# Optimization experiments

Measured on AMD Instinct MI355X. Metric: run time of the kernel, lower is better.

Reference implementation:

```python
import jax, jax.numpy as jnp
import numpy as np

B, N_CAPS, N_VOTES, D_IN, D_H, D_CP = 1024, 64, 36, 256, 128, 32
TWO_PI = 2.0 * np.pi


def geometric_transform(pose):
    # pose: [..., 6] -> affine 3x3 matrix [..., 3, 3] (nonlinear, full affine)
    sx, sy, theta, shear, tx, ty = jnp.split(pose, 6, axis=-1)
    sx = jax.nn.sigmoid(sx) + 1e-2
    sy = jax.nn.sigmoid(sy) + 1e-2
    tx = jnp.tanh(tx * 5.0)
    ty = jnp.tanh(ty * 5.0)
    shear = jnp.tanh(shear * 5.0)
    theta = theta * TWO_PI
    c, s = jnp.cos(theta), jnp.sin(theta)
    row0 = jnp.concatenate([sx * c + shear * sy * s, -sx * s + shear * sy * c, tx], -1)
    row1 = jnp.concatenate([sy * s, sy * c, ty], -1)
    zeros = jnp.zeros_like(tx)
    row2 = jnp.concatenate([zeros, zeros, jnp.ones_like(tx)], -1)
    return jnp.stack([row0, row1, row2], axis=-2)


def setup_inputs() -> dict:
    key = jax.random.key(0)
    ks = jax.random.split(key, 16)
    u = lambda k, shp: 0.5 * (jax.random.uniform(k, shp, jnp.float32) - 0.5)
    return {
        "features": jax.random.normal(ks[0], (B, N_CAPS, D_IN), jnp.float32),
        "w1": u(ks[1], (1, N_CAPS, D_IN, D_H)),
        "b1": jnp.zeros((1, N_CAPS, 1, D_H), jnp.float32),
        "w2": u(ks[2], (1, N_CAPS, D_H, D_CP)),
        "b2": jnp.zeros((1, N_CAPS, 1, D_CP), jnp.float32),
        "caps_mlp_w": u(ks[3], (1, N_CAPS, D_CP + 1, D_H)),
        "caps_mlp_b": jnp.zeros((1, N_CAPS, 1, D_H), jnp.float32),
        "cpr_dynamic_w": u(ks[4], (1, N_CAPS, D_H, N_VOTES * 6)),
        "ccr_w": u(ks[5], (1, N_CAPS, D_H, 6)),
        "ccr_b": jnp.zeros((1, N_CAPS, 1, 6), jnp.float32),
        "pres_caps_w": u(ks[6], (1, N_CAPS, D_H, 1)),
        "pres_caps_b": jnp.zeros((1, N_CAPS, 1, 1), jnp.float32),
        "pres_vote_w": u(ks[7], (1, N_CAPS, D_H, N_VOTES)),
        "pres_vote_b": jnp.zeros((1, N_CAPS, 1, N_VOTES), jnp.float32),
        "scale_vote_w": u(ks[8], (1, N_CAPS, D_H, N_VOTES)),
        "scale_vote_b": jnp.zeros((1, N_CAPS, 1, N_VOTES), jnp.float32),
        "cpr_static": jax.random.uniform(ks[9], (1, N_CAPS, N_VOTES, 6), jnp.float32) - 0.5,
    }


def reference(features, w1, b1, w2, b2, caps_mlp_w, caps_mlp_b, cpr_dynamic_w,
              ccr_w, ccr_b, pres_caps_w, pres_caps_b, pres_vote_w, pres_vote_b,
              scale_vote_w, scale_vote_b, cpr_static):
    batch_size = features.shape[0]
    x = features[:, :, None, :]                               # [B, C, 1, 256]
    h = jax.nn.relu(x @ w1 + b1)                              # [B, C, 1, H]
    raw_caps_params = jax.nn.relu(h @ w2 + b2)                # [B, C, 1, P]
    caps_exist = jnp.ones(raw_caps_params.shape[:-1] + (1,), raw_caps_params.dtype)
    caps_params = jnp.concatenate([raw_caps_params, caps_exist], -1)  # [B, C, 1, P+1]
    caps_feat = jax.nn.relu(caps_params @ caps_mlp_w + caps_mlp_b)    # [B, C, 1, H]

    cpr_dynamic = (caps_feat @ cpr_dynamic_w).reshape(batch_size, N_CAPS, N_VOTES, 6)
    ccr = caps_feat @ ccr_w + ccr_b                           # [B, C, 1, 6]
    pres_logit_per_caps = (caps_feat @ pres_caps_w + pres_caps_b)[:, :, 0, :]   # [B, C, 1]
    pres_logit_per_vote = (caps_feat @ pres_vote_w + pres_vote_b)[:, :, 0, :]   # [B, C, V]
    scale_per_vote = (caps_feat @ scale_vote_w + scale_vote_b)[:, :, 0, :]      # [B, C, V]

    ccr_mat = geometric_transform(ccr)                        # [B, C, 1, 3, 3]
    cpr_mat = geometric_transform(cpr_dynamic + cpr_static)   # [B, C, V, 3, 3]
    votes = ccr_mat @ cpr_mat                                 # [B, C, V, 3, 3]

    pres_per_caps = jax.nn.sigmoid(pres_logit_per_caps)
    pres_per_vote = pres_per_caps * jax.nn.sigmoid(pres_logit_per_vote)
    scale_per_vote = jax.nn.softplus(scale_per_vote + 0.5) + 0.01
    dynamic_weights_l2 = jnp.sum(cpr_dynamic ** 2) / batch_size / 2.0
    return (votes, scale_per_vote, pres_per_vote, pres_logit_per_caps,
            pres_logit_per_vote, dynamic_weights_l2, raw_caps_params[:, :, 0, :], features)
```

## Files before the change

### kernel.cpp

```cpp
#include <hip/hip_runtime.h>
#include <math.h>

#define NB   1024
#define NC   64
#define DIN  256
#define DH   128
#define DCP  32
#define NV   36

#define OFF0 0
#define OFF1 21233664
#define OFF2 23592960
#define OFF3 25952256
#define OFF4 26017792
#define OFF5 28377088
#define OFF6 28377089
#define OFF7 30474241

#define SM_FST 0
#define SM_R2  4224
#define SM_R3  8576
#define SM_TOT 9664

#define SM_XS  SM_R2
#define SM_W1C (SM_R2 + 544)
#define SM_W2S SM_R2
#define SM_WM  SM_R2
#define SM_WH  SM_R2
#define SM_HD  (SM_R2 + 1280)
#define SM_HB  (SM_R2 + 3872)
#define SM_WD  SM_R2
#define SM_DYN SM_R2
#define SM_CPS SM_R3
#define SM_M   SM_R3
#define SM_PSIG (SM_R3 + 192)

__device__ __forceinline__ float sigm(float x) { return 1.0f / (1.0f + __expf(-x)); }
__device__ __forceinline__ float tanh5(float x) {
    x = fminf(fmaxf(5.0f * x, -15.0f), 15.0f);
    float z = __expf(2.0f * x);
    return (z - 1.0f) / (z + 1.0f);
}
__device__ __forceinline__ void geo(const float* p, float* m) {
    float sx = sigm(p[0]) + 0.01f;
    float sy = sigm(p[1]) + 0.01f;
    float th = p[2] * 6.28318530717958647692f;
    float sh = tanh5(p[3]);
    float tx = tanh5(p[4]);
    float ty = tanh5(p[5]);
    float cc = __cosf(th), ss = __sinf(th);
    m[0] =  sx * cc + sh * sy * ss;
    m[1] = -sx * ss + sh * sy * cc;
    m[2] = tx;
    m[3] = sy * ss;
    m[4] = sy * cc;
    m[5] = ty;
}

__global__ void zero_l2_kernel(float* out) { out[OFF5] = 0.0f; }

__global__ __launch_bounds__(256, 4)
void caps_fused_kernel(const float* __restrict__ feat,
                       const float* __restrict__ w1,  const float* __restrict__ b1,
                       const float* __restrict__ w2,  const float* __restrict__ b2,
                       const float* __restrict__ wm,  const float* __restrict__ bm,
                       const float* __restrict__ wdy,
                       const float* __restrict__ wccr,const float* __restrict__ bccr,
                       const float* __restrict__ wpc, const float* __restrict__ bpc,
                       const float* __restrict__ wpv, const float* __restrict__ bpv,
                       const float* __restrict__ wsv, const float* __restrict__ bsv,
                       const float* __restrict__ cst,
                       float* __restrict__ out)
{
    __shared__ float sm[SM_TOT];
    const int t  = threadIdx.x;
    const int c  = blockIdx.y;
    const int rb = blockIdx.x * 32;

    {
        const int tx = t & 31;
        const int ty = t >> 5;
        float acc[4][4] = {};
        const int xrow = t >> 3, xk2 = (t & 7) * 2;
        for (int k0 = 0; k0 < DIN; k0 += 16) {
            __syncthreads();
            {
                const int gi = (rb + xrow) * (NC * DIN) + c * DIN + k0 + xk2;
                const float2 v = *(const float2*)&feat[gi];
                sm[SM_XS + xrow * 17 + xk2]     = v.x;
                sm[SM_XS + xrow * 17 + xk2 + 1] = v.y;
                out[OFF7 + gi]     = v.x;
                out[OFF7 + gi + 1] = v.y;
            }
            *(float4*)&sm[SM_W1C + t * 4] =
                *(const float4*)&w1[c * (DIN * DH) + k0 * DH + t * 4];
            *(float4*)&sm[SM_W1C + (t + 256) * 4] =
                *(const float4*)&w1[c * (DIN * DH) + k0 * DH + (t + 256) * 4];
            __syncthreads();
#pragma unroll
            for (int kk = 0; kk < 16; ++kk) {
                const float a0 = sm[SM_XS + (ty * 4 + 0) * 17 + kk];
                const float a1 = sm[SM_XS + (ty * 4 + 1) * 17 + kk];
                const float a2 = sm[SM_XS + (ty * 4 + 2) * 17 + kk];
                const float a3 = sm[SM_XS + (ty * 4 + 3) * 17 + kk];
                const float4 bv = *(const float4*)&sm[SM_W1C + kk * DH + tx * 4];
                acc[0][0] += a0 * bv.x; acc[0][1] += a0 * bv.y; acc[0][2] += a0 * bv.z; acc[0][3] += a0 * bv.w;
                acc[1][0] += a1 * bv.x; acc[1][1] += a1 * bv.y; acc[1][2] += a1 * bv.z; acc[1][3] += a1 * bv.w;
                acc[2][0] += a2 * bv.x; acc[2][1] += a2 * bv.y; acc[2][2] += a2 * bv.z; acc[2][3] += a2 * bv.w;
                acc[3][0] += a3 * bv.x; acc[3][1] += a3 * bv.y; acc[3][2] += a3 * bv.z; acc[3][3] += a3 * bv.w;
            }
        }
        const float4 bb4 = *(const float4*)&b1[c * DH + tx * 4];
        const float bb[4] = { bb4.x, bb4.y, bb4.z, bb4.w };
#pragma unroll
        for (int i = 0; i < 4; ++i)
#pragma unroll
            for (int j = 0; j < 4; ++j) {
                float v = fmaxf(acc[i][j] + bb[j], 0.0f);
                sm[SM_FST + (tx * 4 + j) * 33 + (ty * 4 + i)] = v;
            }
    }
    __syncthreads();

#pragma unroll
    for (int p = 0; p < 4; ++p) {
        const int idx = t + p * 256;
        *(float4*)&sm[SM_W2S + idx * 4] = *(const float4*)&w2[c * (DH * DCP) + idx * 4];
    }
    __syncthreads();
    {
        const int b  = t & 31;
        const int j4 = (t >> 5) << 2;
        float acc[4] = {};
#pragma unroll 8
        for (int k = 0; k < DH; ++k) {
            const float h = sm[SM_FST + k * 33 + b];
            const float4 wv = *(const float4*)&sm[SM_W2S + k * DCP + j4];
            acc[0] += h * wv.x; acc[1] += h * wv.y; acc[2] += h * wv.z; acc[3] += h * wv.w;
        }
#pragma unroll
        for (int jj = 0; jj < 4; ++jj) {
            const float v = fmaxf(acc[jj] + b2[c * DCP + j4 + jj], 0.0f);
            out[OFF6 + ((rb + b) * NC + c) * DCP + j4 + jj] = v;
            sm[SM_CPS + b * 34 + j4 + jj] = v;
        }
        if (t < 32) sm[SM_CPS + t * 34 + 32] = 1.0f;
    }
    __syncthreads();

#pragma unroll
    for (int p = 0; p < 5; ++p) {
        const int idx = t + p * 256;
        if (idx < 1056)
            *(float4*)&sm[SM_WM + idx * 4] = *(const float4*)&wm[c * (33 * DH) + idx * 4];
    }
    __syncthreads();
    {
        const int b  = t & 31;
        const int nb = (t >> 5) << 4;
        float acc[16] = {};
        for (int k = 0; k < 33; ++k) {
            const float a = sm[SM_CPS + b * 34 + k];
#pragma unroll
            for (int jq = 0; jq < 4; ++jq) {
                const float4 wv = *(const float4*)&sm[SM_WM + k * DH + nb + jq * 4];
                acc[jq*4+0] += a * wv.x; acc[jq*4+1] += a * wv.y;
                acc[jq*4+2] += a * wv.z; acc[jq*4+3] += a * wv.w;
            }
        }
#pragma unroll
        for (int j = 0; j < 16; ++j) {
            const float v = fmaxf(acc[j] + bm[c * DH + nb + j], 0.0f);
            sm[SM_FST + (nb + j) * 33 + b] = v;
        }
    }
    __syncthreads();

    {
        const int txx = t & 15;
        const int tyy = t >> 4;
        float acc[2][5] = {};
        for (int k0 = 0; k0 < DH; k0 += 16) {
            __syncthreads();
#pragma unroll
            for (int p = 0; p < 5; ++p) {
                const int idx = t + p * 256;
                const int kk = idx / 80, col = idx % 80;
                const int kg = k0 + kk;
                float v = 0.0f;
                if (col < 6)        v = wccr[c * (DH * 6) + kg * 6 + col];
                else if (col == 6)  v = wpc[c * DH + kg];
                else if (col < 43)  v = wpv[c * (DH * NV) + kg * NV + (col - 7)];
                else if (col < 79)  v = wsv[c * (DH * NV) + kg * NV + (col - 43)];
                sm[SM_WH + kk * 80 + col] = v;
            }
            if (k0 == 0 && t < 80) {
                float v = 0.0f;
                if (t < 6)       v = bccr[c * 6 + t];
                else if (t == 6) v = bpc[c];
                else if (t < 43) v = bpv[c * NV + (t - 7)];
                else if (t < 79) v = bsv[c * NV + (t - 43)];
                sm[SM_HB + t] = v;
            }
            __syncthreads();
#pragma unroll
            for (int kk = 0; kk < 16; ++kk) {
                const float a0 = sm[SM_FST + (k0 + kk) * 33 + tyy * 2 + 0];
                const float a1 = sm[SM_FST + (k0 + kk) * 33 + tyy * 2 + 1];
#pragma unroll
                for (int j = 0; j < 5; ++j) {
                    const float w = sm[SM_WH + kk * 80 + txx * 5 + j];
                    acc[0][j] += a0 * w;
                    acc[1][j] += a1 * w;
                }
            }
        }
#pragma unroll
        for (int i = 0; i < 2; ++i)
#pragma unroll
            for (int j = 0; j < 5; ++j)
                sm[SM_HD + (tyy * 2 + i) * 81 + txx * 5 + j] = acc[i][j];
    }
    __syncthreads();

    if (t < 32) {
        const int b = t;
        const float plc = sm[SM_HD + b * 81 + 6] + sm[SM_HB + 6];
        out[OFF3 + (rb + b) * NC + c] = plc;
        sm[SM_PSIG + b] = sigm(plc);
        float p[6], m[6];
#pragma unroll
        for (int i = 0; i < 6; ++i) p[i] = sm[SM_HD + b * 81 + i] + sm[SM_HB + i];
        geo(p, m);
#pragma unroll
        for (int i = 0; i < 6; ++i) sm[SM_M + b * 6 + i] = m[i];
    }
    __syncthreads();

#pragma unroll
    for (int p = 0; p < 10; ++p) {
        const int item = t + p * 256;
        const int b = item / 80, col = item % 80;
        if (col >= 7 && col < 79) {
            const float v = sm[SM_HD + b * 81 + col] + sm[SM_HB + col];
            const int base = ((rb + b) * NC + c) * NV;
            if (col < 43) {
                const int o = col - 7;
                out[OFF4 + base + o] = v;
                out[OFF2 + base + o] = sm[SM_PSIG + b] * sigm(v);
            } else {
                const int o = col - 43;
                float sp = v + 0.5f;
                sp = (sp > 15.0f) ? sp : log1pf(__expf(sp));
                out[OFF1 + base + o] = sp + 0.01f;
            }
        }
    }

    float l2loc = 0.0f;
    {
        const int g   = t & 63;
        const int ty4 = t >> 6;
        float acc[8][4] = {};
        for (int k0 = 0; k0 < DH; k0 += 16) {
            __syncthreads();
#pragma unroll
            for (int p = 0; p < 7; ++p) {
                const int i2  = t + p * 256;
                const int col = (i2 * 2) % 224;
                const int row = (i2 * 2) / 224;
                float2 v = make_float2(0.0f, 0.0f);
                if (col < 216)
                    v = *(const float2*)&wdy[c * (DH * 216) + (k0 + row) * 216 + col];
                *(float2*)&sm[SM_WD + row * 224 + col] = v;
            }
            __syncthreads();
#pragma unroll
            for (int kk = 0; kk < 16; ++kk) {
                float a[8];
#pragma unroll
                for (int i = 0; i < 8; ++i)
                    a[i] = sm[SM_FST + (k0 + kk) * 33 + ty4 * 8 + i];
                const float4 w = *(const float4*)&sm[SM_WD + kk * 224 + g * 4];
#pragma unroll
                for (int i = 0; i < 8; ++i) {
                    acc[i][0] += a[i] * w.x; acc[i][1] += a[i] * w.y;
                    acc[i][2] += a[i] * w.z; acc[i][3] += a[i] * w.w;
                }
            }
        }
        for (int half = 0; half < 2; ++half) {
            __syncthreads();
            if (g < 54 && (g >= 27) == (half == 1)) {
#pragma unroll
                for (int i = 0; i < 8; ++i)
#pragma unroll
                    for (int j = 0; j < 4; ++j)
                        sm[SM_DYN + (ty4 * 8 + i) * 109 + (g * 4 + j - half * 108)] = acc[i][j];
            }
            __syncthreads();
#pragma unroll
            for (int p = 0; p < 3; ++p) {
                const int item = t + p * 256;
                if (item < 576) {
                    const int b = item / 18, vh = item % 18;
                    const int v = half * 18 + vh;
                    float dyn[6], pose[6], mB[6];
                    float ss = 0.0f;
#pragma unroll
                    for (int j = 0; j < 6; ++j) {
                        dyn[j] = sm[SM_DYN + b * 109 + vh * 6 + j];
                        ss += dyn[j] * dyn[j];
                        pose[j] = dyn[j] + cst[c * (NV * 6) + v * 6 + j];
                    }
                    l2loc += ss;
                    geo(pose, mB);
                    const float A0 = sm[SM_M + b * 6 + 0], A1 = sm[SM_M + b * 6 + 1];
                    const float A2 = sm[SM_M + b * 6 + 2], A3 = sm[SM_M + b * 6 + 3];
                    const float A4 = sm[SM_M + b * 6 + 4], A5 = sm[SM_M + b * 6 + 5];
                    const int ob = (((rb + b) * NC + c) * NV + v) * 9;
                    out[OFF0 + ob + 0] = A0 * mB[0] + A1 * mB[3];
                    out[OFF0 + ob + 1] = A0 * mB[1] + A1 * mB[4];
                    out[OFF0 + ob + 2] = A0 * mB[2] + A1 * mB[5] + A2;
                    out[OFF0 + ob + 3] = A3 * mB[0] + A4 * mB[3];
                    out[OFF0 + ob + 4] = A3 * mB[1] + A4 * mB[4];
                    out[OFF0 + ob + 5] = A3 * mB[2] + A4 * mB[5] + A5;
                    out[OFF0 + ob + 6] = 0.0f;
                    out[OFF0 + ob + 7] = 0.0f;
                    out[OFF0 + ob + 8] = 1.0f;
                }
            }
        }
    }

    l2loc += __shfl_down(l2loc, 32, 64);
    l2loc += __shfl_down(l2loc, 16, 64);
    l2loc += __shfl_down(l2loc, 8, 64);
    l2loc += __shfl_down(l2loc, 4, 64);
    l2loc += __shfl_down(l2loc, 2, 64);
    l2loc += __shfl_down(l2loc, 1, 64);
    if ((t & 63) == 0) atomicAdd(&out[OFF5], l2loc * (1.0f / 2048.0f));
}

extern "C" void kernel_launch(void* const* d_in, const int* in_sizes, int n_in,
                              void* d_out, int out_size, void* d_ws, size_t ws_size,
                              hipStream_t stream)
{
    const float* feat = (const float*)d_in[0];
    const float* w1   = (const float*)d_in[1];
    const float* b1   = (const float*)d_in[2];
    const float* w2   = (const float*)d_in[3];
    const float* b2   = (const float*)d_in[4];
    const float* wm   = (const float*)d_in[5];
    const float* bm   = (const float*)d_in[6];
    const float* wdy  = (const float*)d_in[7];
    const float* wccr = (const float*)d_in[8];
    const float* bccr = (const float*)d_in[9];
    const float* wpc  = (const float*)d_in[10];
    const float* bpc  = (const float*)d_in[11];
    const float* wpv  = (const float*)d_in[12];
    const float* bpv  = (const float*)d_in[13];
    const float* wsv  = (const float*)d_in[14];
    const float* bsv  = (const float*)d_in[15];
    const float* cst  = (const float*)d_in[16];
    float* out = (float*)d_out;

    zero_l2_kernel<<<1, 1, 0, stream>>>(out);
    dim3 grid(NB / 32, NC);
    caps_fused_kernel<<<grid, 256, 0, stream>>>(feat, w1, b1, w2, b2, wm, bm, wdy,
                                                wccr, bccr, wpc, bpc, wpv, bpv,
                                                wsv, bsv, cst, out);
}
```

Baseline: 622.3 us.

## Use direct global-to-LDS loads, swizzled transposed activations, and vectorized LDS reads

Replaces the register-staged weight copies into shared memory with global_load_lds direct transfers, chunking the W2 and caps-MLP weight loads so they fit a smaller LDS footprint. The activation buffers are stored transposed with an XOR swizzle and stride 36, so GEMM inner loops can use float4/float2 LDS reads instead of scalar loads. The feature pass-through copy is moved into a separate vectorized prologue, and the head weight tile is repacked to 8-wide slots for vector reads. The aim is fewer LDS instructions and bank conflicts, and lower shared-memory use per block. The risk is extra barriers from the chunked loads, plus correctness depending on the async LDS loads completing before the barrier.

```diff
diff --git a/kernel.cpp b/kernel.cpp
--- a/kernel.cpp
+++ b/kernel.cpp
@@ -17,23 +17,32 @@
 #define OFF6 28377089
 #define OFF7 30474241
 
+#define FSTR 36
+#define SWZ(h) ((((h) >> 2) & 7) << 2)
+
 #define SM_FST 0
-#define SM_R2  4224
-#define SM_R3  8576
-#define SM_TOT 9664
-
-#define SM_XS  SM_R2
-#define SM_W1C (SM_R2 + 544)
+#define SM_R2  4608
+#define SM_R3  8192
+#define SM_TOT 9280
+
+#define SM_XT  SM_R2
+#define SM_W1C (SM_R2 + 576)
 #define SM_W2S SM_R2
 #define SM_WM  SM_R2
 #define SM_WH  SM_R2
-#define SM_HD  (SM_R2 + 1280)
-#define SM_HB  (SM_R2 + 3872)
+#define SM_HD  (SM_R2 + 1024)
 #define SM_WD  SM_R2
 #define SM_DYN SM_R2
 #define SM_CPS SM_R3
 #define SM_M   SM_R3
 #define SM_PSIG (SM_R3 + 192)
+#define SM_HB  (SM_R3 + 224)
+
+__device__ __forceinline__ void gload16(const float* g, float* l) {
+    __builtin_amdgcn_global_load_lds(
+        (const __attribute__((address_space(1))) void*)g,
+        (__attribute__((address_space(3))) void*)l, 16, 0, 0);
+}
 
 __device__ __forceinline__ float sigm(float x) { return 1.0f / (1.0f + __expf(-x)); }
 __device__ __forceinline__ float tanh5(float x) {
@@ -72,10 +81,20 @@
                        const float* __restrict__ cst,
                        float* __restrict__ out)
 {
-    __shared__ float sm[SM_TOT];
+    __shared__ __align__(16) float sm[SM_TOT];
     const int t  = threadIdx.x;
     const int c  = blockIdx.y;
     const int rb = blockIdx.x * 32;
+
+#pragma unroll
+    for (int p = 0; p < 8; ++p) {
+        const int idx = t + p * 256;
+        const int row = idx >> 6, c4 = idx & 63;
+        const int gi = (rb + row) * (NC * DIN) + c * DIN + c4 * 4;
+        const float4 v = *(const float4*)&feat[gi];
+        float* o = &out[OFF7 + gi];
+        o[0] = v.x; o[1] = v.y; o[2] = v.z; o[3] = v.w;
+    }
 
     {
         const int tx = t & 31;
@@ -87,56 +106,51 @@
             {
                 const int gi = (rb + xrow) * (NC * DIN) + c * DIN + k0 + xk2;
                 const float2 v = *(const float2*)&feat[gi];
-                sm[SM_XS + xrow * 17 + xk2]     = v.x;
-                sm[SM_XS + xrow * 17 + xk2 + 1] = v.y;
-                out[OFF7 + gi]     = v.x;
-                out[OFF7 + gi + 1] = v.y;
-            }
-            *(float4*)&sm[SM_W1C + t * 4] =
-                *(const float4*)&w1[c * (DIN * DH) + k0 * DH + t * 4];
-            *(float4*)&sm[SM_W1C + (t + 256) * 4] =
-                *(const float4*)&w1[c * (DIN * DH) + k0 * DH + (t + 256) * 4];
+                sm[SM_XT + xk2 * FSTR + (xrow ^ SWZ(xk2))]           = v.x;
+                sm[SM_XT + (xk2 + 1) * FSTR + (xrow ^ SWZ(xk2 + 1))] = v.y;
+            }
+            gload16(&w1[c * (DIN * DH) + k0 * DH + t * 4],        &sm[SM_W1C + t * 4]);
+            gload16(&w1[c * (DIN * DH) + k0 * DH + 1024 + t * 4], &sm[SM_W1C + 1024 + t * 4]);
             __syncthreads();
 #pragma unroll
             for (int kk = 0; kk < 16; ++kk) {
-                const float a0 = sm[SM_XS + (ty * 4 + 0) * 17 + kk];
-                const float a1 = sm[SM_XS + (ty * 4 + 1) * 17 + kk];
-                const float a2 = sm[SM_XS + (ty * 4 + 2) * 17 + kk];
-                const float a3 = sm[SM_XS + (ty * 4 + 3) * 17 + kk];
+                const float4 av = *(const float4*)&sm[SM_XT + kk * FSTR + ((ty * 4) ^ SWZ(kk))];
                 const float4 bv = *(const float4*)&sm[SM_W1C + kk * DH + tx * 4];
-                acc[0][0] += a0 * bv.x; acc[0][1] += a0 * bv.y; acc[0][2] += a0 * bv.z; acc[0][3] += a0 * bv.w;
-                acc[1][0] += a1 * bv.x; acc[1][1] += a1 * bv.y; acc[1][2] += a1 * bv.z; acc[1][3] += a1 * bv.w;
-                acc[2][0] += a2 * bv.x; acc[2][1] += a2 * bv.y; acc[2][2] += a2 * bv.z; acc[2][3] += a2 * bv.w;
-                acc[3][0] += a3 * bv.x; acc[3][1] += a3 * bv.y; acc[3][2] += a3 * bv.z; acc[3][3] += a3 * bv.w;
+                acc[0][0] += av.x * bv.x; acc[0][1] += av.x * bv.y; acc[0][2] += av.x * bv.z; acc[0][3] += av.x * bv.w;
+                acc[1][0] += av.y * bv.x; acc[1][1] += av.y * bv.y; acc[1][2] += av.y * bv.z; acc[1][3] += av.y * bv.w;
+                acc[2][0] += av.z * bv.x; acc[2][1] += av.z * bv.y; acc[2][2] += av.z * bv.z; acc[2][3] += av.z * bv.w;
+                acc[3][0] += av.w * bv.x; acc[3][1] += av.w * bv.y; acc[3][2] += av.w * bv.z; acc[3][3] += av.w * bv.w;
             }
         }
         const float4 bb4 = *(const float4*)&b1[c * DH + tx * 4];
         const float bb[4] = { bb4.x, bb4.y, bb4.z, bb4.w };
-#pragma unroll
-        for (int i = 0; i < 4; ++i)
-#pragma unroll
-            for (int j = 0; j < 4; ++j) {
-                float v = fmaxf(acc[i][j] + bb[j], 0.0f);
-                sm[SM_FST + (tx * 4 + j) * 33 + (ty * 4 + i)] = v;
-            }
-    }
-    __syncthreads();
-
-#pragma unroll
-    for (int p = 0; p < 4; ++p) {
-        const int idx = t + p * 256;
-        *(float4*)&sm[SM_W2S + idx * 4] = *(const float4*)&w2[c * (DH * DCP) + idx * 4];
-    }
-    __syncthreads();
+        const int sH = (tx & 7) * 4;
+#pragma unroll
+        for (int j = 0; j < 4; ++j) {
+            float4 w;
+            w.x = fmaxf(acc[0][j] + bb[j], 0.0f);
+            w.y = fmaxf(acc[1][j] + bb[j], 0.0f);
+            w.z = fmaxf(acc[2][j] + bb[j], 0.0f);
+            w.w = fmaxf(acc[3][j] + bb[j], 0.0f);
+            *(float4*)&sm[SM_FST + (tx * 4 + j) * FSTR + ((ty * 4) ^ sH)] = w;
+        }
+    }
+
     {
         const int b  = t & 31;
         const int j4 = (t >> 5) << 2;
         float acc[4] = {};
-#pragma unroll 8
-        for (int k = 0; k < DH; ++k) {
-            const float h = sm[SM_FST + k * 33 + b];
-            const float4 wv = *(const float4*)&sm[SM_W2S + k * DCP + j4];
-            acc[0] += h * wv.x; acc[1] += h * wv.y; acc[2] += h * wv.z; acc[3] += h * wv.w;
+        for (int k0 = 0; k0 < DH; k0 += 32) {
+            __syncthreads();
+            gload16(&w2[c * (DH * DCP) + k0 * DCP + t * 4], &sm[SM_W2S + t * 4]);
+            __syncthreads();
+#pragma unroll
+            for (int kk = 0; kk < 32; ++kk) {
+                const int k = k0 + kk;
+                const float h = sm[SM_FST + k * FSTR + (b ^ SWZ(k))];
+                const float4 wv = *(const float4*)&sm[SM_W2S + kk * DCP + j4];
+                acc[0] += h * wv.x; acc[1] += h * wv.y; acc[2] += h * wv.z; acc[3] += h * wv.w;
+            }
         }
 #pragma unroll
         for (int jj = 0; jj < 4; ++jj) {
@@ -146,53 +160,56 @@
         }
         if (t < 32) sm[SM_CPS + t * 34 + 32] = 1.0f;
     }
-    __syncthreads();
-
-#pragma unroll
-    for (int p = 0; p < 5; ++p) {
-        const int idx = t + p * 256;
-        if (idx < 1056)
-            *(float4*)&sm[SM_WM + idx * 4] = *(const float4*)&wm[c * (33 * DH) + idx * 4];
-    }
-    __syncthreads();
+
     {
         const int b  = t & 31;
         const int nb = (t >> 5) << 4;
         float acc[16] = {};
-        for (int k = 0; k < 33; ++k) {
-            const float a = sm[SM_CPS + b * 34 + k];
-#pragma unroll
-            for (int jq = 0; jq < 4; ++jq) {
-                const float4 wv = *(const float4*)&sm[SM_WM + k * DH + nb + jq * 4];
-                acc[jq*4+0] += a * wv.x; acc[jq*4+1] += a * wv.y;
-                acc[jq*4+2] += a * wv.z; acc[jq*4+3] += a * wv.w;
+        for (int k0 = 0; k0 < 33; k0 += 11) {
+            __syncthreads();
+            gload16(&wm[c * (33 * DH) + k0 * DH + t * 4], &sm[SM_WM + t * 4]);
+            if (t < 96)
+                gload16(&wm[c * (33 * DH) + k0 * DH + 1024 + t * 4], &sm[SM_WM + 1024 + t * 4]);
+            __syncthreads();
+#pragma unroll
+            for (int kk = 0; kk < 11; ++kk) {
+                const float a = sm[SM_CPS + b * 34 + k0 + kk];
+#pragma unroll
+                for (int jq = 0; jq < 4; ++jq) {
+                    const float4 wv = *(const float4*)&sm[SM_WM + kk * DH + nb + jq * 4];
+                    acc[jq*4+0] += a * wv.x; acc[jq*4+1] += a * wv.y;
+                    acc[jq*4+2] += a * wv.z; acc[jq*4+3] += a * wv.w;
+                }
             }
         }
 #pragma unroll
         for (int j = 0; j < 16; ++j) {
             const float v = fmaxf(acc[j] + bm[c * DH + nb + j], 0.0f);
-            sm[SM_FST + (nb + j) * 33 + b] = v;
-        }
-    }
-    __syncthreads();
+            sm[SM_FST + (nb + j) * FSTR + (b ^ SWZ(nb + j))] = v;
+        }
+    }
 
     {
         const int txx = t & 15;
         const int tyy = t >> 4;
         float acc[2][5] = {};
-        for (int k0 = 0; k0 < DH; k0 += 16) {
-            __syncthreads();
-#pragma unroll
-            for (int p = 0; p < 5; ++p) {
+        for (int k0 = 0; k0 < DH; k0 += 8) {
+            __syncthreads();
+#pragma unroll
+            for (int p = 0; p < 4; ++p) {
                 const int idx = t + p * 256;
-                const int kk = idx / 80, col = idx % 80;
-                const int kg = k0 + kk;
-                float v = 0.0f;
-                if (col < 6)        v = wccr[c * (DH * 6) + kg * 6 + col];
-                else if (col == 6)  v = wpc[c * DH + kg];
-                else if (col < 43)  v = wpv[c * (DH * NV) + kg * NV + (col - 7)];
-                else if (col < 79)  v = wsv[c * (DH * NV) + kg * NV + (col - 43)];
-                sm[SM_WH + kk * 80 + col] = v;
+                const int kk = idx >> 7, slot = idx & 127;
+                const int grp = slot >> 3, j = slot & 7;
+                if (j < 5) {
+                    const int col = grp * 5 + j;
+                    const int kg = k0 + kk;
+                    float v = 0.0f;
+                    if (col < 6)        v = wccr[c * (DH * 6) + kg * 6 + col];
+                    else if (col == 6)  v = wpc[c * DH + kg];
+                    else if (col < 43)  v = wpv[c * (DH * NV) + kg * NV + (col - 7)];
+                    else if (col < 79)  v = wsv[c * (DH * NV) + kg * NV + (col - 43)];
+                    sm[SM_WH + kk * 128 + slot] = v;
+                }
             }
             if (k0 == 0 && t < 80) {
                 float v = 0.0f;
@@ -204,33 +221,33 @@
             }
             __syncthreads();
 #pragma unroll
-            for (int kk = 0; kk < 16; ++kk) {
-                const float a0 = sm[SM_FST + (k0 + kk) * 33 + tyy * 2 + 0];
-                const float a1 = sm[SM_FST + (k0 + kk) * 33 + tyy * 2 + 1];
-#pragma unroll
-                for (int j = 0; j < 5; ++j) {
-                    const float w = sm[SM_WH + kk * 80 + txx * 5 + j];
-                    acc[0][j] += a0 * w;
-                    acc[1][j] += a1 * w;
-                }
+            for (int kk = 0; kk < 8; ++kk) {
+                const int k = k0 + kk;
+                const float2 a2 = *(const float2*)&sm[SM_FST + k * FSTR + ((tyy * 2) ^ SWZ(k))];
+                const float4 w4 = *(const float4*)&sm[SM_WH + kk * 128 + txx * 8];
+                const float  w5 = sm[SM_WH + kk * 128 + txx * 8 + 4];
+                acc[0][0] += a2.x * w4.x; acc[0][1] += a2.x * w4.y; acc[0][2] += a2.x * w4.z;
+                acc[0][3] += a2.x * w4.w; acc[0][4] += a2.x * w5;
+                acc[1][0] += a2.y * w4.x; acc[1][1] += a2.y * w4.y; acc[1][2] += a2.y * w4.z;
+                acc[1][3] += a2.y * w4.w; acc[1][4] += a2.y * w5;
             }
         }
 #pragma unroll
         for (int i = 0; i < 2; ++i)
 #pragma unroll
             for (int j = 0; j < 5; ++j)
-                sm[SM_HD + (tyy * 2 + i) * 81 + txx * 5 + j] = acc[i][j];
+                sm[SM_HD + (tyy * 2 + i) * 80 + txx * 5 + j] = acc[i][j];
     }
     __syncthreads();
 
     if (t < 32) {
         const int b = t;
-        const float plc = sm[SM_HD + b * 81 + 6] + sm[SM_HB + 6];
+        const float plc = sm[SM_HD + b * 80 + 6] + sm[SM_HB + 6];
         out[OFF3 + (rb + b) * NC + c] = plc;
         sm[SM_PSIG + b] = sigm(plc);
         float p[6], m[6];
 #pragma unroll
-        for (int i = 0; i < 6; ++i) p[i] = sm[SM_HD + b * 81 + i] + sm[SM_HB + i];
+        for (int i = 0; i < 6; ++i) p[i] = sm[SM_HD + b * 80 + i] + sm[SM_HB + i];
         geo(p, m);
 #pragma unroll
         for (int i = 0; i < 6; ++i) sm[SM_M + b * 6 + i] = m[i];
@@ -242,7 +259,7 @@
         const int item = t + p * 256;
         const int b = item / 80, col = item % 80;
         if (col >= 7 && col < 79) {
-            const float v = sm[SM_HD + b * 81 + col] + sm[SM_HB + col];
+            const float v = sm[SM_HD + b * 80 + col] + sm[SM_HB + col];
             const int base = ((rb + b) * NC + c) * NV;
             if (col < 43) {
                 const int o = col - 7;
@@ -260,43 +277,46 @@
     float l2loc = 0.0f;
     {
         const int g   = t & 63;
+        const int gc  = min(g, 53);
         const int ty4 = t >> 6;
         float acc[8][4] = {};
         for (int k0 = 0; k0 < DH; k0 += 16) {
             __syncthreads();
-#pragma unroll
-            for (int p = 0; p < 7; ++p) {
-                const int i2  = t + p * 256;
-                const int col = (i2 * 2) % 224;
-                const int row = (i2 * 2) / 224;
-                float2 v = make_float2(0.0f, 0.0f);
-                if (col < 216)
-                    v = *(const float2*)&wdy[c * (DH * 216) + (k0 + row) * 216 + col];
-                *(float2*)&sm[SM_WD + row * 224 + col] = v;
+            {
+                const int gb = c * (DH * 216) + k0 * 216;
+                gload16(&wdy[gb + t * 4],        &sm[SM_WD + t * 4]);
+                gload16(&wdy[gb + 1024 + t * 4], &sm[SM_WD + 1024 + t * 4]);
+                gload16(&wdy[gb + 2048 + t * 4], &sm[SM_WD + 2048 + t * 4]);
+                if (t < 96)
+                    gload16(&wdy[gb + 3072 + t * 4], &sm[SM_WD + 3072 + t * 4]);
             }
             __syncthreads();
 #pragma unroll
             for (int kk = 0; kk < 16; ++kk) {
-                float a[8];
-#pragma unroll
-                for (int i = 0; i < 8; ++i)
-                    a[i] = sm[SM_FST + (k0 + kk) * 33 + ty4 * 8 + i];
-                const float4 w = *(const float4*)&sm[SM_WD + kk * 224 + g * 4];
+                const int k = k0 + kk;
+                const int rbase = (ty4 * 8) ^ SWZ(k);
+                const float4 aA = *(const float4*)&sm[SM_FST + k * FSTR + rbase];
+                const float4 aB = *(const float4*)&sm[SM_FST + k * FSTR + (rbase ^ 4)];
+                const float4 w = *(const float4*)&sm[SM_WD + kk * 216 + gc * 4];
+                acc[0][0] += aA.x * w.x; acc[0][1] += aA.x * w.y; acc[0][2] += aA.x * w.z; acc[0][3] += aA.x * w.w;
+                acc[1][0] += aA.y * w.x; acc[1][1] += aA.y * w.y; acc[1][2] += aA.y * w.z; acc[1][3] += aA.y * w.w;
+                acc[2][0] += aA.z * w.x; acc[2][1] += aA.z * w.y; acc[2][2] += aA.z * w.z; acc[2][3] += aA.z * w.w;
+                acc[3][0] += aA.w * w.x; acc[3][1] += aA.w * w.y; acc[3][2] += aA.w * w.z; acc[3][3] += aA.w * w.w;
+                acc[4][0] += aB.x * w.x; acc[4][1] += aB.x * w.y; acc[4][2] += aB.x * w.z; acc[4][3] += aB.x * w.w;
+                acc[5][0] += aB.y * w.x; acc[5][1] += aB.y * w.y; acc[5][2] += aB.y * w.z; acc[5][3] += aB.y * w.w;
+                acc[6][0] += aB.z * w.x; acc[6][1] += aB.z * w.y; acc[6][2] += aB.z * w.z; acc[6][3] += aB.z * w.w;
+                acc[7][0] += aB.w * w.x; acc[7][1] += aB.w * w.y; acc[7][2] += aB.w * w.z; acc[7][3] += aB.w * w.w;
+            }
+        }
+        for (int half = 0; half < 2; ++half) {
+            __syncthreads();
+            if (g < 54 && (g >= 27) == (half == 1)) {
+                const int cg = g * 4 - half * 108;
 #pragma unroll
                 for (int i = 0; i < 8; ++i) {
-                    acc[i][0] += a[i] * w.x; acc[i][1] += a[i] * w.y;
-                    acc[i][2] += a[i] * w.z; acc[i][3] += a[i] * w.w;
+                    float4 v; v.x = acc[i][0]; v.y = acc[i][1]; v.z = acc[i][2]; v.w = acc[i][3];
+                    *(float4*)&sm[SM_DYN + (ty4 * 8 + i) * 112 + cg] = v;
                 }
-            }
-        }
-        for (int half = 0; half < 2; ++half) {
-            __syncthreads();
-            if (g < 54 && (g >= 27) == (half == 1)) {
-#pragma unroll
-                for (int i = 0; i < 8; ++i)
-#pragma unroll
-                    for (int j = 0; j < 4; ++j)
-                        sm[SM_DYN + (ty4 * 8 + i) * 109 + (g * 4 + j - half * 108)] = acc[i][j];
             }
             __syncthreads();
 #pragma unroll
@@ -309,7 +329,7 @@
                     float ss = 0.0f;
 #pragma unroll
                     for (int j = 0; j < 6; ++j) {
-                        dyn[j] = sm[SM_DYN + b * 109 + vh * 6 + j];
+                        dyn[j] = sm[SM_DYN + b * 112 + vh * 6 + j];
                         ss += dyn[j] * dyn[j];
                         pose[j] = dyn[j] + cst[c * (NV * 6) + v * 6 + j];
                     }
```

New measurement: 778.4 us. +25.1%, slower.
